# Kernel tuning notes

Hardware: AMD Instinct MI355X
Metric: run time of the kernel (lower is better)

The kernel has to match this reference:

```python
import jax, jax.numpy as jnp
import numpy as np

NUM_HEADS = 16
KERNEL_SIZE = 13  # odd, neighborhood size nh = 6


def setup_inputs() -> dict:
    key = jax.random.key(0)
    ks = jax.random.split(key, 6)
    B, L, C = 4, 4096, 512
    return {
        "x": jax.random.normal(ks[0], (B, L, C), dtype=jnp.float32),
        "qkv_w": jax.random.normal(ks[1], (3 * C, C), dtype=jnp.float32) * (C ** -0.5),
        "qkv_b": jax.random.normal(ks[2], (3 * C,), dtype=jnp.float32) * 0.02,
        "rpb": jax.random.normal(ks[3], (NUM_HEADS, 2 * KERNEL_SIZE - 1), dtype=jnp.float32) * 0.02,
        "proj_w": jax.random.normal(ks[4], (C, C), dtype=jnp.float32) * (C ** -0.5),
        "proj_b": jax.random.normal(ks[5], (C,), dtype=jnp.float32) * 0.02,
    }


def reference(x, qkv_w, qkv_b, rpb, proj_w, proj_b):
    B, L, C = x.shape
    H, K = NUM_HEADS, KERNEL_SIZE
    Dh = C // H
    scale = Dh ** -0.5
    nh = K // 2

    # qkv projection (torch Linear: x @ W.T + b)
    qkv = (x @ qkv_w.T + qkv_b).reshape(B, L, 3, H, Dh)
    qkv = jnp.transpose(qkv, (2, 0, 3, 1, 4))  # (3, B, H, L, Dh)
    q, k, v = qkv[0] * scale, qkv[1], qkv[2]

    # neighborhood indices: window of K keys, shifted (not clipped) at borders
    pos = jnp.arange(L)
    start = jnp.clip(pos - nh, 0, L - K)            # (L,)
    idx = start[:, None] + jnp.arange(K)[None, :]   # (L, K) key positions
    # relative-position-bias index: (key_pos - query_pos) + (K-1), in [0, 2K-2]
    bias_idx = idx - pos[:, None] + (K - 1)         # (L, K)

    k_g = k[:, :, idx, :]                           # (B, H, L, K, Dh)
    attn = jnp.einsum('bhld,bhlkd->bhlk', q, k_g)   # (B, H, L, K)
    attn = attn + rpb[:, bias_idx][None]            # add (H, L, K) bias
    attn = jax.nn.softmax(attn, axis=-1)

    v_g = v[:, :, idx, :]                           # (B, H, L, K, Dh)
    out = jnp.einsum('bhlk,bhlkd->bhld', attn, v_g)  # (B, H, L, Dh)
    out = jnp.transpose(out, (0, 2, 1, 3)).reshape(B, L, C)
    return out @ proj_w.T + proj_b
```

## Files before the change

kernel.cpp:

```cpp
#include <hip/hip_runtime.h>
#include <hip/hip_bf16.h>

#define BATCH   4
#define LSEQ    4096
#define CCH     512
#define HNUM    16
#define DH      32
#define KSZ     13
#define NHALF   6
#define M_TOT   16384
#define N_QKV   1536
#define KDIM    512
#define BK      64

typedef __attribute__((ext_vector_type(8))) short  short8;
typedef __attribute__((ext_vector_type(4))) short  short4_t;
typedef __attribute__((ext_vector_type(4))) float  float4_t;

__device__ __forceinline__ unsigned short f32_to_bf16(float f) {
    union { float f; unsigned int u; } un; un.f = f;
    unsigned int u = un.u;
    u += 0x7FFFu + ((u >> 16) & 1u);
    return (unsigned short)(u >> 16);
}
__device__ __forceinline__ float bf16_to_f32(unsigned short h) {
    union { unsigned int u; float f; } un; un.u = ((unsigned int)h) << 16;
    return un.f;
}

__device__ __forceinline__ void gload_lds16(const unsigned short* g, unsigned short* l) {
    __builtin_amdgcn_global_load_lds(
        (const __attribute__((address_space(1))) unsigned int*)g,
        (__attribute__((address_space(3))) unsigned int*)l,
        16, 0, 0);
}

__global__ void cvt_f32_bf16_v4(const float4_t* __restrict__ in,
                                short4_t* __restrict__ out, int n4) {
    int i = blockIdx.x * blockDim.x + threadIdx.x;
    int stride = gridDim.x * blockDim.x;
    for (; i < n4; i += stride) {
        float4_t v = in[i];
        short4_t h;
        h.x = (short)f32_to_bf16(v.x);
        h.y = (short)f32_to_bf16(v.y);
        h.z = (short)f32_to_bf16(v.z);
        h.w = (short)f32_to_bf16(v.w);
        out[i] = h;
    }
}

__global__ __launch_bounds__(512, 2) void gemm_qkv(
    const unsigned short* __restrict__ Xb,
    const unsigned short* __restrict__ W,
    const float* __restrict__ bias,
    unsigned short* __restrict__ qkvout)
{
    extern __shared__ __align__(16) unsigned short lds[];
    const int tid  = threadIdx.x;
    const int wv   = tid >> 6, ln = tid & 63;

    const int wg   = blockIdx.x;
    const int swz  = (wg & 7) * 48 + (wg >> 3);
    const int m0   = (swz & 63) * 256;
    const int n0   = (swz >> 6) * 256;

    const int wm   = (wv >> 2) * 128;
    const int wn   = (wv & 3) * 64;
    const int lr   = ln & 15;
    const int lg   = ln >> 4;
    const int rgrp = ln >> 3;
    const int csw  = ((ln & 7) ^ rgrp) * 8;

    float4_t acc[8][4];
    #pragma unroll
    for (int m = 0; m < 8; ++m)
        #pragma unroll
        for (int n = 0; n < 4; ++n)
            acc[m][n] = (float4_t){0.f, 0.f, 0.f, 0.f};

    #define STAGE(t_, buf_) do {                                              \
        const int k0_ = (t_) * BK;                                            \
        _Pragma("unroll")                                                     \
        for (int c4 = 0; c4 < 4; ++c4) {                                      \
            int r_ = wv * 32 + c4 * 8;                                        \
            gload_lds16(Xb + (size_t)(m0 + r_ + rgrp) * KDIM + k0_ + csw,     \
                        &lds[(buf_) * 16384 + r_ * 64]);                      \
            gload_lds16(W  + (size_t)(n0 + r_ + rgrp) * KDIM + k0_ + csw,     \
                        &lds[32768 + (buf_) * 16384 + r_ * 64]);              \
        }                                                                     \
    } while (0)

    STAGE(0, 0);

    #pragma unroll 2
    for (int t = 0; t < 8; ++t) {
        const int buf = t & 1;
        if (t < 7) {
            STAGE(t + 1, buf ^ 1);
            asm volatile("s_waitcnt vmcnt(8)" ::: "memory");
        } else {
            asm volatile("s_waitcnt vmcnt(0)" ::: "memory");
        }
        __builtin_amdgcn_s_barrier();

        const unsigned short* Ab = &lds[buf * 16384];
        const unsigned short* Bb = &lds[32768 + buf * 16384];

        short8 af[2][4], bf[2][2];
        #pragma unroll
        for (int qm = 0; qm < 2; ++qm) {
            #pragma unroll
            for (int kk = 0; kk < 2; ++kk)
                #pragma unroll
                for (int m = 0; m < 4; ++m) {
                    int row = wm + qm * 64 + m * 16 + lr;
                    int c   = (kk * 4 + lg) ^ (lr & 7);
                    af[kk][m] = *reinterpret_cast<const short8*>(&Ab[row * 64 + c * 8]);
                }
            #pragma unroll
            for (int qn = 0; qn < 2; ++qn) {
                #pragma unroll
                for (int kk = 0; kk < 2; ++kk)
                    #pragma unroll
                    for (int n = 0; n < 2; ++n) {
                        int row = wn + qn * 32 + n * 16 + lr;
                        int c   = (kk * 4 + lg) ^ (lr & 7);
                        bf[kk][n] = *reinterpret_cast<const short8*>(&Bb[row * 64 + c * 8]);
                    }
                __builtin_amdgcn_s_barrier();
                __builtin_amdgcn_sched_barrier(0);
                __builtin_amdgcn_s_setprio(1);
                #pragma unroll
                for (int kk = 0; kk < 2; ++kk)
                    #pragma unroll
                    for (int m = 0; m < 4; ++m)
                        #pragma unroll
                        for (int n = 0; n < 2; ++n)
                            acc[qm * 4 + m][qn * 2 + n] =
                                __builtin_amdgcn_mfma_f32_16x16x32_bf16(
                                    af[kk][m], bf[kk][n],
                                    acc[qm * 4 + m][qn * 2 + n], 0, 0, 0);
                __builtin_amdgcn_s_setprio(0);
            }
        }
    }
    #undef STAGE

    const float qscale = 0.17677669529663687f;
    #pragma unroll
    for (int mf = 0; mf < 8; ++mf) {
        #pragma unroll
        for (int nf = 0; nf < 4; ++nf) {
            int gn    = n0 + wn + nf * 16 + lr;
            int which = gn >> 9;
            int hh    = (gn >> 5) & 15;
            int dd    = gn & 31;
            float bsv = bias[gn];
            #pragma unroll
            for (int r = 0; r < 4; ++r) {
                int gm = m0 + wm + mf * 16 + lg * 4 + r;
                float v = acc[mf][nf][r] + bsv;
                if (which == 0) v *= qscale;
                int b_ = gm >> 12, l = gm & 4095;
                size_t off = (((size_t)which * BATCH + b_) * HNUM + hh) *
                                 ((size_t)LSEQ * DH) + (size_t)l * DH + dd;
                qkvout[off] = f32_to_bf16(v);
            }
        }
    }
}

__global__ __launch_bounds__(256) void natten_fwd(
    const unsigned short* __restrict__ qkv,
    const float* __restrict__ rpb,
    unsigned short* __restrict__ ctx)
{
    __shared__ __align__(16) unsigned short ks[4 * 268 * 8];
    __shared__ __align__(16) unsigned short vs[4 * 268 * 8];
    __shared__ float rpb_s[2 * KSZ - 1];

    const int t    = threadIdx.x;
    const int lblk = blockIdx.x & 15;
    const int bh   = blockIdx.x >> 4;
    const int hh   = bh & 15, b_ = bh >> 4;
    const int l0   = lblk * 256;

    const int r0    = max(l0 - NHALF, 0);
    const int rend  = min(l0 + 256 + NHALF, LSEQ);
    const int nrows = rend - r0;

    const size_t plane = (size_t)LSEQ * DH;
    const size_t kbase = (((size_t)1 * BATCH + b_) * HNUM + hh) * plane;
    const size_t vbase = (((size_t)2 * BATCH + b_) * HNUM + hh) * plane;

    {
        const int cq  = t >> 6;
        const int rr  = t & 63;
        #pragma unroll
        for (int base = 0; base < 320; base += 64) {
            int row = base + rr;
            if (row < nrows) {
                *reinterpret_cast<short8*>(&ks[(cq * 268 + row) * 8]) =
                    *reinterpret_cast<const short8*>(&qkv[kbase + (size_t)(r0 + row) * DH + cq * 8]);
                *reinterpret_cast<short8*>(&vs[(cq * 268 + row) * 8]) =
                    *reinterpret_cast<const short8*>(&qkv[vbase + (size_t)(r0 + row) * DH + cq * 8]);
            }
        }
    }
    if (t < 2 * KSZ - 1) rpb_s[t] = rpb[hh * (2 * KSZ - 1) + t];
    __syncthreads();

    const int l = l0 + t;
    float q[DH];
    const size_t qoff = (((size_t)0 * BATCH + b_) * HNUM + hh) * plane + (size_t)l * DH;
    #pragma unroll
    for (int cq = 0; cq < 4; ++cq) {
        short8 qv = *reinterpret_cast<const short8*>(&qkv[qoff + cq * 8]);
        #pragma unroll
        for (int e = 0; e < 8; ++e) q[cq * 8 + e] = bf16_to_f32((unsigned short)qv[e]);
    }

    const int start = min(max(l - NHALF, 0), LSEQ - KSZ);
    float logit[KSZ];
    #pragma unroll
    for (int j = 0; j < KSZ; ++j) {
        int kr = start + j - r0;
        float s = 0.f;
        #pragma unroll
        for (int cq = 0; cq < 4; ++cq) {
            short8 kv = *reinterpret_cast<const short8*>(&ks[(cq * 268 + kr) * 8]);
            #pragma unroll
            for (int e = 0; e < 8; ++e)
                s += q[cq * 8 + e] * bf16_to_f32((unsigned short)kv[e]);
        }
        logit[j] = s + rpb_s[start + j - l + (KSZ - 1)];
    }
    float mx = logit[0];
    #pragma unroll
    for (int j = 1; j < KSZ; ++j) mx = fmaxf(mx, logit[j]);
    float p[KSZ], sum = 0.f;
    #pragma unroll
    for (int j = 0; j < KSZ; ++j) { p[j] = __expf(logit[j] - mx); sum += p[j]; }
    const float inv = 1.f / sum;

    float o[DH];
    #pragma unroll
    for (int d = 0; d < DH; ++d) o[d] = 0.f;
    #pragma unroll
    for (int j = 0; j < KSZ; ++j) {
        int kr = start + j - r0;
        float pj = p[j] * inv;
        #pragma unroll
        for (int cq = 0; cq < 4; ++cq) {
            short8 vv = *reinterpret_cast<const short8*>(&vs[(cq * 268 + kr) * 8]);
            #pragma unroll
            for (int e = 0; e < 8; ++e)
                o[cq * 8 + e] += pj * bf16_to_f32((unsigned short)vv[e]);
        }
    }
    const size_t obase = ((size_t)(b_ * LSEQ + l)) * CCH + hh * DH;
    #pragma unroll
    for (int cq = 0; cq < 4; ++cq) {
        short8 ov;
        #pragma unroll
        for (int e = 0; e < 8; ++e) ov[e] = (short)f32_to_bf16(o[cq * 8 + e]);
        *reinterpret_cast<short8*>(&ctx[obase + cq * 8]) = ov;
    }
}

__global__ __launch_bounds__(256) void gemm_proj(
    const unsigned short* __restrict__ Xb,
    const unsigned short* __restrict__ W,
    const float* __restrict__ bias,
    float* __restrict__ out)
{
    __shared__ __align__(16) unsigned short As[128 * BK];
    __shared__ __align__(16) unsigned short Bs[128 * BK];
    const int tid  = threadIdx.x;
    const int wv   = tid >> 6, ln = tid & 63;
    const int m0   = blockIdx.x * 128;
    const int n0   = blockIdx.y * 128;
    const int wm   = (wv >> 1) * 64;
    const int wn   = (wv & 1) * 64;
    const int lr   = ln & 15;
    const int lg   = ln >> 4;
    const int rgrp = ln >> 3;
    const int csw  = ((ln & 7) ^ rgrp) * 8;

    float4_t acc[4][4];
    #pragma unroll
    for (int m = 0; m < 4; ++m)
        #pragma unroll
        for (int n = 0; n < 4; ++n)
            acc[m][n] = (float4_t){0.f, 0.f, 0.f, 0.f};

    for (int k0 = 0; k0 < KDIM; k0 += BK) {
        #pragma unroll
        for (int it = 0; it < 4; ++it) {
            int ch  = it * 4 + wv;
            int row = ch * 8 + rgrp;
            gload_lds16(Xb + (size_t)(m0 + row) * KDIM + k0 + csw,
                        &As[ch * 8 * BK]);
            gload_lds16(W  + (size_t)(n0 + row) * KDIM + k0 + csw,
                        &Bs[ch * 8 * BK]);
        }
        __syncthreads();
        short8 af[2][4], bfr[2][4];
        #pragma unroll
        for (int kk = 0; kk < 2; ++kk) {
            #pragma unroll
            for (int m = 0; m < 4; ++m) {
                int row = wm + m * 16 + lr;
                int c   = (kk * 4 + lg) ^ (row & 7);
                af[kk][m] = *reinterpret_cast<const short8*>(&As[row * BK + c * 8]);
            }
            #pragma unroll
            for (int n = 0; n < 4; ++n) {
                int row = wn + n * 16 + lr;
                int c   = (kk * 4 + lg) ^ (row & 7);
                bfr[kk][n] = *reinterpret_cast<const short8*>(&Bs[row * BK + c * 8]);
            }
        }
        #pragma unroll
        for (int kk = 0; kk < 2; ++kk)
            #pragma unroll
            for (int m = 0; m < 4; ++m)
                #pragma unroll
                for (int n = 0; n < 4; ++n)
                    acc[m][n] = __builtin_amdgcn_mfma_f32_16x16x32_bf16(
                        af[kk][m], bfr[kk][n], acc[m][n], 0, 0, 0);
        __syncthreads();
    }

    #pragma unroll
    for (int m = 0; m < 4; ++m) {
        #pragma unroll
        for (int n = 0; n < 4; ++n) {
            int gn = n0 + wn + n * 16 + lr;
            float bsv = bias[gn];
            #pragma unroll
            for (int r = 0; r < 4; ++r) {
                int gm = m0 + wm + m * 16 + lg * 4 + r;
                out[(size_t)gm * CCH + gn] = acc[m][n][r] + bsv;
            }
        }
    }
}

extern "C" void kernel_launch(void* const* d_in, const int* in_sizes, int n_in,
                              void* d_out, int out_size, void* d_ws, size_t ws_size,
                              hipStream_t stream) {
    const float* x      = (const float*)d_in[0];
    const float* qkv_w  = (const float*)d_in[1];
    const float* qkv_b  = (const float*)d_in[2];
    const float* rpb    = (const float*)d_in[3];
    const float* proj_w = (const float*)d_in[4];
    const float* proj_b = (const float*)d_in[5];
    float* out = (float*)d_out;
    char* ws = (char*)d_ws;

    unsigned short* qkv = (unsigned short*)(ws);
    unsigned short* xb  = (unsigned short*)(ws + 50331648);
    unsigned short* ctx = (unsigned short*)(ws + 50331648);
    unsigned short* wq  = (unsigned short*)(ws + 67108864);
    unsigned short* wp  = (unsigned short*)(ws + 68681728);

    cvt_f32_bf16_v4<<<2048, 256, 0, stream>>>((const float4_t*)x, (short4_t*)xb, M_TOT * KDIM / 4);
    cvt_f32_bf16_v4<<<768, 256, 0, stream>>>((const float4_t*)qkv_w, (short4_t*)wq, 786432 / 4);
    cvt_f32_bf16_v4<<<256, 256, 0, stream>>>((const float4_t*)proj_w, (short4_t*)wp, 262144 / 4);

    gemm_qkv<<<384, 512, 131072, stream>>>(xb, wq, qkv_b, qkv);

    natten_fwd<<<BATCH * HNUM * (LSEQ / 256), 256, 0, stream>>>(qkv, rpb, ctx);

    dim3 g2(M_TOT / 128, CCH / 128);
    gemm_proj<<<g2, 256, 0, stream>>>(ctx, wp, proj_b, out);
}
```

Baseline: 91.49 us.

## Triple-buffer both GEMMs with 32-wide K tiles and enlarge the projection tile

Both bf16 GEMMs move to a three-buffer LDS pipeline with K tiles of 32. Each buffer stores 16-row slabs in lane order, so the MFMA fragment reads need no XOR swizzle. Each loop step has one barrier and a vmcnt wait, and it prefetches two tiles ahead to hide global-to-LDS latency. The projection GEMM changes from 128x128 tiles with 256 threads to 256x128 tiles with 512 threads, using a swizzled block order and dynamic LDS. The QKV kernel drops to one block per CU in its launch bounds, trading occupancy for deeper prefetch and a larger register budget. Halving the K tile doubles the number of loop steps and barriers.

New measurement: 102.7 us. 1.12x slower.

```diff
diff --git a/kernel.cpp b/kernel.cpp
--- a/kernel.cpp
+++ b/kernel.cpp
@@ -11,7 +11,7 @@
 #define M_TOT   16384
 #define N_QKV   1536
 #define KDIM    512
-#define BK      64
+#define BKQ     32
 
 typedef __attribute__((ext_vector_type(8))) short  short8;
 typedef __attribute__((ext_vector_type(4))) short  short4_t;
@@ -50,7 +50,7 @@
     }
 }
 
-__global__ __launch_bounds__(512, 2) void gemm_qkv(
+__global__ __launch_bounds__(512, 1) void gemm_qkv(
     const unsigned short* __restrict__ Xb,
     const unsigned short* __restrict__ W,
     const float* __restrict__ bias,
@@ -69,8 +69,8 @@
     const int wn   = (wv & 3) * 64;
     const int lr   = ln & 15;
     const int lg   = ln >> 4;
-    const int rgrp = ln >> 3;
-    const int csw  = ((ln & 7) ^ rgrp) * 8;
+    const int srow = ln & 15;
+    const int schk = (ln >> 4) * 8;
 
     float4_t acc[8][4];
     #pragma unroll
@@ -79,73 +79,70 @@
         for (int n = 0; n < 4; ++n)
             acc[m][n] = (float4_t){0.f, 0.f, 0.f, 0.f};
 
-    #define STAGE(t_, buf_) do {                                              \
-        const int k0_ = (t_) * BK;                                            \
-        _Pragma("unroll")                                                     \
-        for (int c4 = 0; c4 < 4; ++c4) {                                      \
-            int r_ = wv * 32 + c4 * 8;                                        \
-            gload_lds16(Xb + (size_t)(m0 + r_ + rgrp) * KDIM + k0_ + csw,     \
-                        &lds[(buf_) * 16384 + r_ * 64]);                      \
-            gload_lds16(W  + (size_t)(n0 + r_ + rgrp) * KDIM + k0_ + csw,     \
-                        &lds[32768 + (buf_) * 16384 + r_ * 64]);              \
+    #define STAGE(kt_, base_) do {                                            \
+        const int k0_ = (kt_) * BKQ;                                          \
+        _Pragma("unroll")                                                     \
+        for (int i_ = 0; i_ < 2; ++i_) {                                      \
+            int s_ = i_ * 8 + wv;                                             \
+            gload_lds16(Xb + (size_t)(m0 + s_ * 16 + srow) * KDIM + k0_ + schk,\
+                        (base_) + s_ * 512);                                  \
+        }                                                                     \
+        _Pragma("unroll")                                                     \
+        for (int i_ = 0; i_ < 2; ++i_) {                                      \
+            int s_ = i_ * 8 + wv;                                             \
+            gload_lds16(W + (size_t)(n0 + s_ * 16 + srow) * KDIM + k0_ + schk, \
+                        (base_) + 8192 + s_ * 512);                           \
         }                                                                     \
     } while (0)
 
-    STAGE(0, 0);
-
-    #pragma unroll 2
-    for (int t = 0; t < 8; ++t) {
-        const int buf = t & 1;
-        if (t < 7) {
-            STAGE(t + 1, buf ^ 1);
-            asm volatile("s_waitcnt vmcnt(8)" ::: "memory");
-        } else {
-            asm volatile("s_waitcnt vmcnt(0)" ::: "memory");
-        }
+    #define COMPUTE(base_) do {                                               \
+        const unsigned short* Ab_ = (base_);                                  \
+        const unsigned short* Bb_ = (base_) + 8192;                           \
+        short8 bf_[4];                                                        \
+        _Pragma("unroll")                                                     \
+        for (int n_ = 0; n_ < 4; ++n_)                                        \
+            bf_[n_] = *reinterpret_cast<const short8*>(                       \
+                &Bb_[((wn >> 4) + n_) * 512 + lg * 128 + lr * 8]);            \
+        _Pragma("unroll")                                                     \
+        for (int qm_ = 0; qm_ < 2; ++qm_) {                                   \
+            short8 af_[4];                                                    \
+            _Pragma("unroll")                                                 \
+            for (int m_ = 0; m_ < 4; ++m_)                                    \
+                af_[m_] = *reinterpret_cast<const short8*>(                   \
+                    &Ab_[((wm >> 4) + qm_ * 4 + m_) * 512 + lg * 128 + lr * 8]);\
+            __builtin_amdgcn_s_setprio(1);                                    \
+            _Pragma("unroll")                                                 \
+            for (int m_ = 0; m_ < 4; ++m_)                                    \
+                _Pragma("unroll")                                             \
+                for (int n_ = 0; n_ < 4; ++n_)                                \
+                    acc[qm_ * 4 + m_][n_] =                                   \
+                        __builtin_amdgcn_mfma_f32_16x16x32_bf16(              \
+                            af_[m_], bf_[n_], acc[qm_ * 4 + m_][n_], 0, 0, 0);\
+            __builtin_amdgcn_s_setprio(0);                                    \
+        }                                                                     \
+    } while (0)
+
+    unsigned short* bc = lds;
+    unsigned short* b1 = lds + 16384;
+    unsigned short* b2 = lds + 32768;
+
+    STAGE(0, bc);
+    STAGE(1, b1);
+
+    for (int t = 0; t < 15; ++t) {
+        asm volatile("s_waitcnt vmcnt(4)" ::: "memory");
         __builtin_amdgcn_s_barrier();
-
-        const unsigned short* Ab = &lds[buf * 16384];
-        const unsigned short* Bb = &lds[32768 + buf * 16384];
-
-        short8 af[2][4], bf[2][2];
-        #pragma unroll
-        for (int qm = 0; qm < 2; ++qm) {
-            #pragma unroll
-            for (int kk = 0; kk < 2; ++kk)
-                #pragma unroll
-                for (int m = 0; m < 4; ++m) {
-                    int row = wm + qm * 64 + m * 16 + lr;
-                    int c   = (kk * 4 + lg) ^ (lr & 7);
-                    af[kk][m] = *reinterpret_cast<const short8*>(&Ab[row * 64 + c * 8]);
-                }
-            #pragma unroll
-            for (int qn = 0; qn < 2; ++qn) {
-                #pragma unroll
-                for (int kk = 0; kk < 2; ++kk)
-                    #pragma unroll
-                    for (int n = 0; n < 2; ++n) {
-                        int row = wn + qn * 32 + n * 16 + lr;
-                        int c   = (kk * 4 + lg) ^ (lr & 7);
-                        bf[kk][n] = *reinterpret_cast<const short8*>(&Bb[row * 64 + c * 8]);
-                    }
-                __builtin_amdgcn_s_barrier();
-                __builtin_amdgcn_sched_barrier(0);
-                __builtin_amdgcn_s_setprio(1);
-                #pragma unroll
-                for (int kk = 0; kk < 2; ++kk)
-                    #pragma unroll
-                    for (int m = 0; m < 4; ++m)
-                        #pragma unroll
-                        for (int n = 0; n < 2; ++n)
-                            acc[qm * 4 + m][qn * 2 + n] =
-                                __builtin_amdgcn_mfma_f32_16x16x32_bf16(
-                                    af[kk][m], bf[kk][n],
-                                    acc[qm * 4 + m][qn * 2 + n], 0, 0, 0);
-                __builtin_amdgcn_s_setprio(0);
-            }
-        }
-    }
+        __builtin_amdgcn_sched_barrier(0);
+        if (t < 14) STAGE(t + 2, b2);
+        COMPUTE(bc);
+        unsigned short* tmp = bc; bc = b1; b1 = b2; b2 = tmp;
+    }
+    asm volatile("s_waitcnt vmcnt(0)" ::: "memory");
+    __builtin_amdgcn_s_barrier();
+    __builtin_amdgcn_sched_barrier(0);
+    COMPUTE(bc);
     #undef STAGE
+    #undef COMPUTE
 
     const float qscale = 0.17677669529663687f;
     #pragma unroll
@@ -269,24 +266,27 @@
     }
 }
 
-__global__ __launch_bounds__(256) void gemm_proj(
+__global__ __launch_bounds__(512, 1) void gemm_proj(
     const unsigned short* __restrict__ Xb,
     const unsigned short* __restrict__ W,
     const float* __restrict__ bias,
     float* __restrict__ out)
 {
-    __shared__ __align__(16) unsigned short As[128 * BK];
-    __shared__ __align__(16) unsigned short Bs[128 * BK];
+    extern __shared__ __align__(16) unsigned short lds[];
     const int tid  = threadIdx.x;
     const int wv   = tid >> 6, ln = tid & 63;
-    const int m0   = blockIdx.x * 128;
-    const int n0   = blockIdx.y * 128;
+
+    const int wg   = blockIdx.x;
+    const int swz  = (wg & 7) * 32 + (wg >> 3);
+    const int m0   = (swz & 63) * 256;
+    const int n0   = (swz >> 6) * 128;
+
     const int wm   = (wv >> 1) * 64;
     const int wn   = (wv & 1) * 64;
     const int lr   = ln & 15;
     const int lg   = ln >> 4;
-    const int rgrp = ln >> 3;
-    const int csw  = ((ln & 7) ^ rgrp) * 8;
+    const int srow = ln & 15;
+    const int schk = (ln >> 4) * 8;
 
     float4_t acc[4][4];
     #pragma unroll
@@ -295,54 +295,72 @@
         for (int n = 0; n < 4; ++n)
             acc[m][n] = (float4_t){0.f, 0.f, 0.f, 0.f};
 
-    for (int k0 = 0; k0 < KDIM; k0 += BK) {
-        #pragma unroll
-        for (int it = 0; it < 4; ++it) {
-            int ch  = it * 4 + wv;
-            int row = ch * 8 + rgrp;
-            gload_lds16(Xb + (size_t)(m0 + row) * KDIM + k0 + csw,
-                        &As[ch * 8 * BK]);
-            gload_lds16(W  + (size_t)(n0 + row) * KDIM + k0 + csw,
-                        &Bs[ch * 8 * BK]);
-        }
-        __syncthreads();
-        short8 af[2][4], bfr[2][4];
-        #pragma unroll
-        for (int kk = 0; kk < 2; ++kk) {
-            #pragma unroll
-            for (int m = 0; m < 4; ++m) {
-                int row = wm + m * 16 + lr;
-                int c   = (kk * 4 + lg) ^ (row & 7);
-                af[kk][m] = *reinterpret_cast<const short8*>(&As[row * BK + c * 8]);
-            }
-            #pragma unroll
-            for (int n = 0; n < 4; ++n) {
-                int row = wn + n * 16 + lr;
-                int c   = (kk * 4 + lg) ^ (row & 7);
-                bfr[kk][n] = *reinterpret_cast<const short8*>(&Bs[row * BK + c * 8]);
-            }
-        }
-        #pragma unroll
-        for (int kk = 0; kk < 2; ++kk)
-            #pragma unroll
-            for (int m = 0; m < 4; ++m)
-                #pragma unroll
-                for (int n = 0; n < 4; ++n)
-                    acc[m][n] = __builtin_amdgcn_mfma_f32_16x16x32_bf16(
-                        af[kk][m], bfr[kk][n], acc[m][n], 0, 0, 0);
-        __syncthreads();
-    }
-
-    #pragma unroll
-    for (int m = 0; m < 4; ++m) {
-        #pragma unroll
-        for (int n = 0; n < 4; ++n) {
-            int gn = n0 + wn + n * 16 + lr;
+    #define STAGEP(kt_, base_) do {                                           \
+        const int k0_ = (kt_) * BKQ;                                          \
+        _Pragma("unroll")                                                     \
+        for (int i_ = 0; i_ < 2; ++i_) {                                      \
+            int s_ = i_ * 8 + wv;                                             \
+            gload_lds16(Xb + (size_t)(m0 + s_ * 16 + srow) * KDIM + k0_ + schk,\
+                        (base_) + s_ * 512);                                  \
+        }                                                                     \
+        gload_lds16(W + (size_t)(n0 + wv * 16 + srow) * KDIM + k0_ + schk,    \
+                    (base_) + 8192 + wv * 512);                               \
+    } while (0)
+
+    #define COMPUTEP(base_) do {                                              \
+        const unsigned short* Ab_ = (base_);                                  \
+        const unsigned short* Bb_ = (base_) + 8192;                           \
+        short8 af_[4], bf_[4];                                                \
+        _Pragma("unroll")                                                     \
+        for (int n_ = 0; n_ < 4; ++n_)                                        \
+            bf_[n_] = *reinterpret_cast<const short8*>(                       \
+                &Bb_[((wn >> 4) + n_) * 512 + lg * 128 + lr * 8]);            \
+        _Pragma("unroll")                                                     \
+        for (int m_ = 0; m_ < 4; ++m_)                                        \
+            af_[m_] = *reinterpret_cast<const short8*>(                       \
+                &Ab_[((wm >> 4) + m_) * 512 + lg * 128 + lr * 8]);            \
+        __builtin_amdgcn_s_setprio(1);                                        \
+        _Pragma("unroll")                                                     \
+        for (int m_ = 0; m_ < 4; ++m_)                                        \
+            _Pragma("unroll")                                                 \
+            for (int n_ = 0; n_ < 4; ++n_)                                    \
+                acc[m_][n_] = __builtin_amdgcn_mfma_f32_16x16x32_bf16(        \
+                    af_[m_], bf_[n_], acc[m_][n_], 0, 0, 0);                  \
+        __builtin_amdgcn_s_setprio(0);                                        \
+    } while (0)
+
+    unsigned short* bc = lds;
+    unsigned short* b1 = lds + 12288;
+    unsigned short* b2 = lds + 24576;
+
+    STAGEP(0, bc);
+    STAGEP(1, b1);
+
+    for (int t = 0; t < 15; ++t) {
+        asm volatile("s_waitcnt vmcnt(3)" ::: "memory");
+        __builtin_amdgcn_s_barrier();
+        __builtin_amdgcn_sched_barrier(0);
+        if (t < 14) STAGEP(t + 2, b2);
+        COMPUTEP(bc);
+        unsigned short* tmp = bc; bc = b1; b1 = b2; b2 = tmp;
+    }
+    asm volatile("s_waitcnt vmcnt(0)" ::: "memory");
+    __builtin_amdgcn_s_barrier();
+    __builtin_amdgcn_sched_barrier(0);
+    COMPUTEP(bc);
+    #undef STAGEP
+    #undef COMPUTEP
+
+    #pragma unroll
+    for (int mf = 0; mf < 4; ++mf) {
+        #pragma unroll
+        for (int nf = 0; nf < 4; ++nf) {
+            int gn = n0 + wn + nf * 16 + lr;
             float bsv = bias[gn];
             #pragma unroll
             for (int r = 0; r < 4; ++r) {
-                int gm = m0 + wm + m * 16 + lg * 4 + r;
-                out[(size_t)gm * CCH + gn] = acc[m][n][r] + bsv;
+                int gm = m0 + wm + mf * 16 + lg * 4 + r;
+                out[(size_t)gm * CCH + gn] = acc[mf][nf][r] + bsv;
             }
         }
     }
@@ -370,10 +388,9 @@
     cvt_f32_bf16_v4<<<768, 256, 0, stream>>>((const float4_t*)qkv_w, (short4_t*)wq, 786432 / 4);
     cvt_f32_bf16_v4<<<256, 256, 0, stream>>>((const float4_t*)proj_w, (short4_t*)wp, 262144 / 4);
 
-    gemm_qkv<<<384, 512, 131072, stream>>>(xb, wq, qkv_b, qkv);
+    gemm_qkv<<<384, 512, 98304, stream>>>(xb, wq, qkv_b, qkv);
 
     natten_fwd<<<BATCH * HNUM * (LSEQ / 256), 256, 0, stream>>>(qkv, rpb, ctx);
 
-    dim3 g2(M_TOT / 128, CCH / 128);
-    gemm_proj<<<g2, 256, 0, stream>>>(ctx, wp, proj_b, out);
-}
+    gemm_proj<<<256, 512, 73728, stream>>>(ctx, wp, proj_b, out);
+}
```
